# Kernel tuning notes

Measured on AMD Instinct MI355X. Metric: run time of the kernel, lower is better.

## Reference

```python
import jax, jax.numpy as jnp
import numpy as np

N_NODES = 100000
N_EDGES = 640000
HIDDEN = 128
OUT = 128


def _graph_conv(x, edge_index, W_rel, b_rel, W_root):
    # PyG GraphConv (aggr='add'):
    #   out[i] = x[i] @ W_root.T + (sum_{(j->i) in E} x[j]) @ W_rel.T + b_rel
    src, dst = edge_index[0], edge_index[1]
    agg = jax.ops.segment_sum(x[src], dst, num_segments=N_NODES)  # [N, d_in]
    return x @ W_root.T + agg @ W_rel.T + b_rel


def setup_inputs() -> dict:
    key = jax.random.key(0)
    ks = jax.random.split(key, 10)
    x = jax.random.normal(ks[0], (N_NODES, HIDDEN), dtype=jnp.float32)
    edge_index = jax.random.randint(ks[1], (2, N_EDGES), 0, N_NODES, dtype=jnp.int64)
    s = 1.0 / np.sqrt(HIDDEN)
    def w(k, o, i):
        return jax.random.normal(k, (o, i), dtype=jnp.float32) * s
    return {
        "x": x,
        "edge_index": edge_index,
        "W_rel0": w(ks[2], HIDDEN, HIDDEN), "b0": jnp.zeros((HIDDEN,), jnp.float32), "W_root0": w(ks[3], HIDDEN, HIDDEN),
        "W_rel1": w(ks[4], HIDDEN, HIDDEN), "b1": jnp.zeros((HIDDEN,), jnp.float32), "W_root1": w(ks[5], HIDDEN, HIDDEN),
        "W_rel2": w(ks[6], OUT, HIDDEN),    "b2": jnp.zeros((OUT,), jnp.float32),    "W_root2": w(ks[7], OUT, HIDDEN),
    }


def reference(x, edge_index, W_rel0, b0, W_root0, W_rel1, b1, W_root1, W_rel2, b2, W_root2):
    h = jax.nn.relu(_graph_conv(x, edge_index, W_rel0, b0, W_root0))
    h = jax.nn.relu(_graph_conv(h, edge_index, W_rel1, b1, W_root1))
    h = _graph_conv(h, edge_index, W_rel2, b2, W_root2)  # no ReLU on end_conv
    return h
```

## Files before the change

### kernel.cpp

```cpp
#include <hip/hip_runtime.h>

constexpr int HID = 128;

typedef __attribute__((ext_vector_type(8))) short bf16x8;
typedef __attribute__((ext_vector_type(4))) float f32x4;

__device__ __forceinline__ unsigned short f2bf(float f) {
    unsigned int u = __float_as_uint(f);
    u += 0x7fffu + ((u >> 16) & 1u);
    return (unsigned short)(u >> 16);
}
__device__ __forceinline__ float bf_lo(unsigned int v) { return __uint_as_float(v << 16); }
__device__ __forceinline__ float bf_hi(unsigned int v) { return __uint_as_float(v & 0xffff0000u); }

__device__ __forceinline__ void gload16(const void* g, void* l) {
    __builtin_amdgcn_global_load_lds(
        (const __attribute__((address_space(1))) void*)g,
        (__attribute__((address_space(3))) void*)l, 16, 0, 0);
}

__global__ __launch_bounds__(256) void cvt_x_k(
    const float* __restrict__ in, unsigned short* __restrict__ out, int n4)
{
    const int i = blockIdx.x * 256 + threadIdx.x;
    if (i >= n4) return;
    const float4 v = reinterpret_cast<const float4*>(in)[i];
    ushort4 o;
    o.x = f2bf(v.x); o.y = f2bf(v.y); o.z = f2bf(v.z); o.w = f2bf(v.w);
    reinterpret_cast<ushort4*>(out)[i] = o;
}

struct WPtrs { const float* s[6]; unsigned short* d[6]; };
__global__ __launch_bounds__(256) void cvt_w_k(WPtrs p)
{
    const int which = blockIdx.y;
    const int i = blockIdx.x * 256 + threadIdx.x;
    if (i >= (HID * HID) / 4) return;
    const float4 v = reinterpret_cast<const float4*>(p.s[which])[i];
    ushort4 o;
    o.x = f2bf(v.x); o.y = f2bf(v.y); o.z = f2bf(v.z); o.w = f2bf(v.w);
    reinterpret_cast<ushort4*>(p.d[which])[i] = o;
}

__global__ __launch_bounds__(256) void hist_k(
    const int* __restrict__ dst, int* __restrict__ deg, int nEdges)
{
    const int i = blockIdx.x * blockDim.x + threadIdx.x;
    if (i < nEdges) atomicAdd(&deg[dst[i]], 1);
}

__global__ __launch_bounds__(256) void scan1_k(
    const int* __restrict__ deg, int* __restrict__ part,
    int* __restrict__ blockSums, int n)
{
    __shared__ int s[256];
    const int t = threadIdx.x;
    const int i = blockIdx.x * 1024 + t * 4;
    const int e0 = (i + 0 < n) ? deg[i + 0] : 0;
    const int e1 = (i + 1 < n) ? deg[i + 1] : 0;
    const int e2 = (i + 2 < n) ? deg[i + 2] : 0;
    const int e3 = (i + 3 < n) ? deg[i + 3] : 0;
    const int local = e0 + e1 + e2 + e3;
    s[t] = local;
    __syncthreads();
    for (int off = 1; off < 256; off <<= 1) {
        int v = 0;
        if (t >= off) v = s[t - off];
        __syncthreads();
        if (t >= off) s[t] += v;
        __syncthreads();
    }
    const int incl = s[t];
    int excl = incl - local;
    if (t == 255) blockSums[blockIdx.x] = incl;
    if (i + 0 < n) part[i + 0] = excl; excl += e0;
    if (i + 1 < n) part[i + 1] = excl; excl += e1;
    if (i + 2 < n) part[i + 2] = excl; excl += e2;
    if (i + 3 < n) part[i + 3] = excl;
}

__global__ __launch_bounds__(128) void scan2_k(int* __restrict__ blockSums, int nb)
{
    __shared__ int s[128];
    const int t = threadIdx.x;
    const int v = (t < nb) ? blockSums[t] : 0;
    s[t] = v;
    __syncthreads();
    for (int off = 1; off < 128; off <<= 1) {
        int u = 0;
        if (t >= off) u = s[t - off];
        __syncthreads();
        if (t >= off) s[t] += u;
        __syncthreads();
    }
    if (t < nb) blockSums[t] = s[t] - v;
}

__global__ __launch_bounds__(256) void scan3_k(
    const int* __restrict__ part, const int* __restrict__ blockSums,
    int* __restrict__ rowStart, int* __restrict__ cursor, int n, int nEdges)
{
    const int i = blockIdx.x * blockDim.x + threadIdx.x;
    if (i < n) {
        const int v = part[i] + blockSums[i >> 10];
        rowStart[i] = v;
        cursor[i]   = v;
    }
    if (i == n) rowStart[n] = nEdges;
}

__global__ __launch_bounds__(256) void fill_k(
    const int* __restrict__ src, const int* __restrict__ dst,
    int* __restrict__ cursor, int* __restrict__ eSrc, int nEdges)
{
    const int i = blockIdx.x * blockDim.x + threadIdx.x;
    if (i < nEdges) {
        const int pos = atomicAdd(&cursor[dst[i]], 1);
        eSrc[pos] = src[i];
    }
}

__global__ __launch_bounds__(256) void gather_agg_k(
    const unsigned short* __restrict__ feat,
    const int*            __restrict__ rowStart,
    const int*            __restrict__ eSrc,
    unsigned short*       __restrict__ agg,
    int nNodes)
{
    const int node = (int)((blockIdx.x * blockDim.x + threadIdx.x) >> 6);
    if (node >= nNodes) return;
    const int lane = threadIdx.x & 63;
    const int beg = rowStart[node];
    const int end = rowStart[node + 1];
    const size_t colOff = (size_t)lane * 2;

    float ax = 0.f, ay = 0.f;

    for (int base = beg; base < end; base += 64) {
        const int cnt = min(64, end - base);
        const int si = eSrc[base + min(lane, cnt - 1)];

        int j = 0;
        for (; j + 8 <= cnt; j += 8) {
            unsigned int v[8];
#pragma unroll
            for (int q = 0; q < 8; ++q) {
                const int s = __shfl(si, j + q, 64);
                v[q] = *reinterpret_cast<const unsigned int*>(feat + (size_t)s * HID + colOff);
            }
#pragma unroll
            for (int q = 0; q < 8; ++q) { ax += bf_lo(v[q]); ay += bf_hi(v[q]); }
        }
        if (j + 4 <= cnt) {
            unsigned int v[4];
#pragma unroll
            for (int q = 0; q < 4; ++q) {
                const int s = __shfl(si, j + q, 64);
                v[q] = *reinterpret_cast<const unsigned int*>(feat + (size_t)s * HID + colOff);
            }
#pragma unroll
            for (int q = 0; q < 4; ++q) { ax += bf_lo(v[q]); ay += bf_hi(v[q]); }
            j += 4;
        }
        if (j + 2 <= cnt) {
            const int s0 = __shfl(si, j, 64);
            const int s1 = __shfl(si, j + 1, 64);
            const unsigned int v0 = *reinterpret_cast<const unsigned int*>(feat + (size_t)s0 * HID + colOff);
            const unsigned int v1 = *reinterpret_cast<const unsigned int*>(feat + (size_t)s1 * HID + colOff);
            ax += bf_lo(v0) + bf_lo(v1);
            ay += bf_hi(v0) + bf_hi(v1);
            j += 2;
        }
        if (j < cnt) {
            const int s = __shfl(si, j, 64);
            const unsigned int v = *reinterpret_cast<const unsigned int*>(feat + (size_t)s * HID + colOff);
            ax += bf_lo(v);
            ay += bf_hi(v);
        }
    }

    const unsigned int packed = (unsigned int)f2bf(ax) | ((unsigned int)f2bf(ay) << 16);
    *reinterpret_cast<unsigned int*>(agg + (size_t)node * HID + colOff) = packed;
}

__device__ __forceinline__ void stage_tile(
    const unsigned short* __restrict__ F, const unsigned short* __restrict__ Wm,
    unsigned short* XsBuf, unsigned short* WsBuf,
    int w, int stHalf, int rsub, int srcColB, int k0, int row0, int rowMax)
{
    if (w < 2) {
#pragma unroll
        for (int q = 0; q < 8; ++q) {
            const int row = stHalf * 64 + q * 8 + rsub;
            const int gr  = min(row0 + row, rowMax);
            gload16((const char*)(F + (size_t)gr * HID + k0) + srcColB,
                    XsBuf + (stHalf * 64 + q * 8) * 64);
        }
    } else {
#pragma unroll
        for (int q = 0; q < 8; ++q) {
            const int row = stHalf * 64 + q * 8 + rsub;
            gload16((const char*)(Wm + (size_t)row * HID + k0) + srcColB,
                    WsBuf + (stHalf * 64 + q * 8) * 64);
        }
    }
}

template <int MODE>
__global__ __launch_bounds__(256) void gemm_mfma_k(
    const unsigned short* __restrict__ X,
    const unsigned short* __restrict__ AGG,
    const unsigned short* __restrict__ Wroot,
    const unsigned short* __restrict__ Wrel,
    const float*          __restrict__ bias,
    void*                 __restrict__ OUTv,
    int nRows)
{
    __shared__ unsigned short Xs[2][128 * 64];
    __shared__ unsigned short Ws[2][128 * 64];

    const int tid  = threadIdx.x;
    const int lane = tid & 63;
    const int w    = tid >> 6;
    const int row0 = blockIdx.x * 128;

    const int wr = w >> 1, wc = w & 1;
    const int R0 = wr * 64, C0 = wc * 64;
    const int lr = lane & 15, lk = lane >> 4;
    const int swz = (lr & 7) << 4;

    const int rsub    = lane >> 3;
    const int srcColB = (((lane & 7) ^ rsub) << 4);
    const int stHalf  = w & 1;
    const int rowMax  = nRows - 1;

    f32x4 acc[4][4];
#pragma unroll
    for (int m = 0; m < 4; ++m)
#pragma unroll
        for (int n = 0; n < 4; ++n) acc[m][n] = f32x4{0.f, 0.f, 0.f, 0.f};

    stage_tile(X, Wroot, Xs[0], Ws[0], w, stHalf, rsub, srcColB, 0, row0, rowMax);

#pragma unroll
    for (int t = 0; t < 4; ++t) {
        const int cur = t & 1;
        if (t < 3) {
            const unsigned short* Fn = (t + 1 < 2) ? X : AGG;
            const unsigned short* Wn = (t + 1 < 2) ? Wroot : Wrel;
            stage_tile(Fn, Wn, Xs[cur ^ 1], Ws[cur ^ 1],
                       w, stHalf, rsub, srcColB, ((t + 1) & 1) * 64, row0, rowMax);
            asm volatile("s_waitcnt vmcnt(8)" ::: "memory");
        } else {
            asm volatile("s_waitcnt vmcnt(0)" ::: "memory");
        }
        __builtin_amdgcn_s_barrier();

#pragma unroll
        for (int ks = 0; ks < 2; ++ks) {
            bf16x8 af[4], bfr[4];
            const int kB = (ks * 64 + lk * 16) ^ swz;
#pragma unroll
            for (int m = 0; m < 4; ++m) {
                const int row = R0 + m * 16 + lr;
                af[m] = *reinterpret_cast<const bf16x8*>((const char*)Xs[cur] + row * 128 + kB);
            }
#pragma unroll
            for (int n = 0; n < 4; ++n) {
                const int col = C0 + n * 16 + lr;
                bfr[n] = *reinterpret_cast<const bf16x8*>((const char*)Ws[cur] + col * 128 + kB);
            }
#pragma unroll
            for (int m = 0; m < 4; ++m)
#pragma unroll
                for (int n = 0; n < 4; ++n)
                    acc[m][n] = __builtin_amdgcn_mfma_f32_16x16x32_bf16(
                        af[m], bfr[n], acc[m][n], 0, 0, 0);
        }
        if (t < 3) __builtin_amdgcn_s_barrier();
    }

    float bv[4];
#pragma unroll
    for (int n = 0; n < 4; ++n) bv[n] = bias[C0 + n * 16 + lr];

#pragma unroll
    for (int m = 0; m < 4; ++m) {
        const int rbase = row0 + R0 + m * 16 + lk * 4;
#pragma unroll
        for (int j = 0; j < 4; ++j) {
            const int r = rbase + j;
            if (r < nRows) {
#pragma unroll
                for (int n = 0; n < 4; ++n) {
                    const int col = C0 + n * 16 + lr;
                    float v = acc[m][n][j] + bv[n];
                    if (MODE == 0) {
                        v = fmaxf(v, 0.f);
                        ((unsigned short*)OUTv)[(size_t)r * HID + col] = f2bf(v);
                    } else {
                        ((float*)OUTv)[(size_t)r * HID + col] = v;
                    }
                }
            }
        }
    }
}

extern "C" void kernel_launch(void* const* d_in, const int* in_sizes, int n_in,
                              void* d_out, int out_size, void* d_ws, size_t ws_size,
                              hipStream_t stream)
{
    const float* x      = (const float*)d_in[0];
    const int*   ei     = (const int*)  d_in[1];
    const float* Wrel0  = (const float*)d_in[2];
    const float* b0     = (const float*)d_in[3];
    const float* Wroot0 = (const float*)d_in[4];
    const float* Wrel1  = (const float*)d_in[5];
    const float* b1     = (const float*)d_in[6];
    const float* Wroot1 = (const float*)d_in[7];
    const float* Wrel2  = (const float*)d_in[8];
    const float* b2     = (const float*)d_in[9];
    const float* Wroot2 = (const float*)d_in[10];

    const int nNodes = in_sizes[0] / HID;
    const int nEdges = in_sizes[1] / 2;
    const int* srcI = ei;
    const int* dstI = ei + nEdges;
    const size_t nF = (size_t)nNodes * HID;

    float* OUT = (float*)d_out;

    unsigned short* xb   = (unsigned short*)d_ws;
    unsigned short* hA   = xb + nF;
    unsigned short* hB   = hA + nF;
    unsigned short* aggb = hB + nF;
    unsigned short* wb   = aggb + nF;
    int* deg       = (int*)(wb + 6 * HID * HID);
    int* part      = deg + nNodes;
    int* rowStart  = part + nNodes;
    int* cursor    = rowStart + nNodes + 1;
    int* blockSums = cursor + nNodes;
    int* eSrc      = blockSums + 128;

    unsigned short* Wrel0b  = wb + 0 * HID * HID;
    unsigned short* Wroot0b = wb + 1 * HID * HID;
    unsigned short* Wrel1b  = wb + 2 * HID * HID;
    unsigned short* Wroot1b = wb + 3 * HID * HID;
    unsigned short* Wrel2b  = wb + 4 * HID * HID;
    unsigned short* Wroot2b = wb + 5 * HID * HID;

    cvt_x_k<<<(int)((nF / 4 + 255) / 256), 256, 0, stream>>>(x, xb, (int)(nF / 4));
    WPtrs wp;
    wp.s[0] = Wrel0;  wp.d[0] = Wrel0b;
    wp.s[1] = Wroot0; wp.d[1] = Wroot0b;
    wp.s[2] = Wrel1;  wp.d[2] = Wrel1b;
    wp.s[3] = Wroot1; wp.d[3] = Wroot1b;
    wp.s[4] = Wrel2;  wp.d[4] = Wrel2b;
    wp.s[5] = Wroot2; wp.d[5] = Wroot2b;
    cvt_w_k<<<dim3(16, 6), 256, 0, stream>>>(wp);

    const int nb = (nNodes + 1023) / 1024;
    hipMemsetAsync(deg, 0, (size_t)nNodes * sizeof(int), stream);
    hist_k<<<(nEdges + 255) / 256, 256, 0, stream>>>(dstI, deg, nEdges);
    scan1_k<<<nb, 256, 0, stream>>>(deg, part, blockSums, nNodes);
    scan2_k<<<1, 128, 0, stream>>>(blockSums, nb);
    scan3_k<<<(nNodes + 256) / 256, 256, 0, stream>>>(part, blockSums, rowStart, cursor, nNodes, nEdges);
    fill_k<<<(nEdges + 255) / 256, 256, 0, stream>>>(srcI, dstI, cursor, eSrc, nEdges);

    const int aGrid = (int)(((size_t)nNodes * 64 + 255) / 256);
    const int gGrid = (nNodes + 127) / 128;

    gather_agg_k<<<aGrid, 256, 0, stream>>>(xb, rowStart, eSrc, aggb, nNodes);
    gemm_mfma_k<0><<<gGrid, 256, 0, stream>>>(xb, aggb, Wroot0b, Wrel0b, b0, hA, nNodes);

    gather_agg_k<<<aGrid, 256, 0, stream>>>(hA, rowStart, eSrc, aggb, nNodes);
    gemm_mfma_k<0><<<gGrid, 256, 0, stream>>>(hA, aggb, Wroot1b, Wrel1b, b1, hB, nNodes);

    gather_agg_k<<<aGrid, 256, 0, stream>>>(hB, rowStart, eSrc, aggb, nNodes);
    gemm_mfma_k<1><<<gGrid, 256, 0, stream>>>(hB, aggb, Wroot2b, Wrel2b, b2, OUT, nNodes);
}
```

Measured before the change: 244.4 us.

## Gather with 16-lane groups and 16-byte loads; record edge rank during histogram

The aggregation kernel now assigns four nodes per wavefront, each handled by a 16-lane group that loads 16-byte chunks (8 bf16 values) per lane. The old layout had one node per wavefront with 4-byte loads. This is meant to cut load instruction count and idle lanes for low-degree nodes. CSR construction now records each edge's atomic rank in the histogram pass, so the fill pass writes without a second atomic. The trade-off is an extra rank array in memory and more registers per lane for accumulators.

```diff
diff --git a/kernel.cpp b/kernel.cpp
--- a/kernel.cpp
+++ b/kernel.cpp
@@ -42,11 +42,12 @@
     reinterpret_cast<ushort4*>(p.d[which])[i] = o;
 }
 
-__global__ __launch_bounds__(256) void hist_k(
-    const int* __restrict__ dst, int* __restrict__ deg, int nEdges)
+__global__ __launch_bounds__(256) void hist_rank_k(
+    const int* __restrict__ dst, int* __restrict__ deg,
+    int* __restrict__ rank, int nEdges)
 {
     const int i = blockIdx.x * blockDim.x + threadIdx.x;
-    if (i < nEdges) atomicAdd(&deg[dst[i]], 1);
+    if (i < nEdges) rank[i] = atomicAdd(&deg[dst[i]], 1);
 }
 
 __global__ __launch_bounds__(256) void scan1_k(
@@ -98,26 +99,20 @@
 
 __global__ __launch_bounds__(256) void scan3_k(
     const int* __restrict__ part, const int* __restrict__ blockSums,
-    int* __restrict__ rowStart, int* __restrict__ cursor, int n, int nEdges)
+    int* __restrict__ rowStart, int n, int nEdges)
 {
     const int i = blockIdx.x * blockDim.x + threadIdx.x;
-    if (i < n) {
-        const int v = part[i] + blockSums[i >> 10];
-        rowStart[i] = v;
-        cursor[i]   = v;
-    }
+    if (i < n) rowStart[i] = part[i] + blockSums[i >> 10];
     if (i == n) rowStart[n] = nEdges;
 }
 
-__global__ __launch_bounds__(256) void fill_k(
+__global__ __launch_bounds__(256) void fill2_k(
     const int* __restrict__ src, const int* __restrict__ dst,
-    int* __restrict__ cursor, int* __restrict__ eSrc, int nEdges)
+    const int* __restrict__ rank, const int* __restrict__ rowStart,
+    int* __restrict__ eSrc, int nEdges)
 {
     const int i = blockIdx.x * blockDim.x + threadIdx.x;
-    if (i < nEdges) {
-        const int pos = atomicAdd(&cursor[dst[i]], 1);
-        eSrc[pos] = src[i];
-    }
+    if (i < nEdges) eSrc[rowStart[dst[i]] + rank[i]] = src[i];
 }
 
 __global__ __launch_bounds__(256) void gather_agg_k(
@@ -127,60 +122,90 @@
     unsigned short*       __restrict__ agg,
     int nNodes)
 {
-    const int node = (int)((blockIdx.x * blockDim.x + threadIdx.x) >> 6);
+    const int wid  = (blockIdx.x * blockDim.x + threadIdx.x) >> 6;
+    const int lane = threadIdx.x & 63;
+    const int g    = lane >> 4;
+    const int sl   = lane & 15;
+    const int node = wid * 4 + g;
     if (node >= nNodes) return;
-    const int lane = threadIdx.x & 63;
+
     const int beg = rowStart[node];
     const int end = rowStart[node + 1];
-    const size_t colOff = (size_t)lane * 2;
-
-    float ax = 0.f, ay = 0.f;
-
-    for (int base = beg; base < end; base += 64) {
-        const int cnt = min(64, end - base);
-        const int si = eSrc[base + min(lane, cnt - 1)];
+    const size_t colOff = (size_t)sl * 8;
+    const int gbase = g << 4;
+
+    float acc[8];
+#pragma unroll
+    for (int q = 0; q < 8; ++q) acc[q] = 0.f;
+
+    for (int base = beg; base < end; base += 16) {
+        const int cnt = min(16, end - base);
+        const int si = eSrc[base + min(sl, cnt - 1)];
 
         int j = 0;
         for (; j + 8 <= cnt; j += 8) {
-            unsigned int v[8];
+            uint4 v[8];
 #pragma unroll
             for (int q = 0; q < 8; ++q) {
-                const int s = __shfl(si, j + q, 64);
-                v[q] = *reinterpret_cast<const unsigned int*>(feat + (size_t)s * HID + colOff);
-            }
-#pragma unroll
-            for (int q = 0; q < 8; ++q) { ax += bf_lo(v[q]); ay += bf_hi(v[q]); }
+                const int s = __shfl(si, gbase + j + q, 64);
+                v[q] = *reinterpret_cast<const uint4*>(feat + (size_t)s * HID + colOff);
+            }
+#pragma unroll
+            for (int q = 0; q < 8; ++q) {
+                acc[0] += bf_lo(v[q].x); acc[1] += bf_hi(v[q].x);
+                acc[2] += bf_lo(v[q].y); acc[3] += bf_hi(v[q].y);
+                acc[4] += bf_lo(v[q].z); acc[5] += bf_hi(v[q].z);
+                acc[6] += bf_lo(v[q].w); acc[7] += bf_hi(v[q].w);
+            }
         }
         if (j + 4 <= cnt) {
-            unsigned int v[4];
+            uint4 v[4];
 #pragma unroll
             for (int q = 0; q < 4; ++q) {
-                const int s = __shfl(si, j + q, 64);
-                v[q] = *reinterpret_cast<const unsigned int*>(feat + (size_t)s * HID + colOff);
-            }
-#pragma unroll
-            for (int q = 0; q < 4; ++q) { ax += bf_lo(v[q]); ay += bf_hi(v[q]); }
+                const int s = __shfl(si, gbase + j + q, 64);
+                v[q] = *reinterpret_cast<const uint4*>(feat + (size_t)s * HID + colOff);
+            }
+#pragma unroll
+            for (int q = 0; q < 4; ++q) {
+                acc[0] += bf_lo(v[q].x); acc[1] += bf_hi(v[q].x);
+                acc[2] += bf_lo(v[q].y); acc[3] += bf_hi(v[q].y);
+                acc[4] += bf_lo(v[q].z); acc[5] += bf_hi(v[q].z);
+                acc[6] += bf_lo(v[q].w); acc[7] += bf_hi(v[q].w);
+            }
             j += 4;
         }
         if (j + 2 <= cnt) {
-            const int s0 = __shfl(si, j, 64);
-            const int s1 = __shfl(si, j + 1, 64);
-            const unsigned int v0 = *reinterpret_cast<const unsigned int*>(feat + (size_t)s0 * HID + colOff);
-            const unsigned int v1 = *reinterpret_cast<const unsigned int*>(feat + (size_t)s1 * HID + colOff);
-            ax += bf_lo(v0) + bf_lo(v1);
-            ay += bf_hi(v0) + bf_hi(v1);
+            uint4 v[2];
+#pragma unroll
+            for (int q = 0; q < 2; ++q) {
+                const int s = __shfl(si, gbase + j + q, 64);
+                v[q] = *reinterpret_cast<const uint4*>(feat + (size_t)s * HID + colOff);
+            }
+#pragma unroll
+            for (int q = 0; q < 2; ++q) {
+                acc[0] += bf_lo(v[q].x); acc[1] += bf_hi(v[q].x);
+                acc[2] += bf_lo(v[q].y); acc[3] += bf_hi(v[q].y);
+                acc[4] += bf_lo(v[q].z); acc[5] += bf_hi(v[q].z);
+                acc[6] += bf_lo(v[q].w); acc[7] += bf_hi(v[q].w);
+            }
             j += 2;
         }
         if (j < cnt) {
-            const int s = __shfl(si, j, 64);
-            const unsigned int v = *reinterpret_cast<const unsigned int*>(feat + (size_t)s * HID + colOff);
-            ax += bf_lo(v);
-            ay += bf_hi(v);
-        }
-    }
-
-    const unsigned int packed = (unsigned int)f2bf(ax) | ((unsigned int)f2bf(ay) << 16);
-    *reinterpret_cast<unsigned int*>(agg + (size_t)node * HID + colOff) = packed;
+            const int s = __shfl(si, gbase + j, 64);
+            const uint4 v = *reinterpret_cast<const uint4*>(feat + (size_t)s * HID + colOff);
+            acc[0] += bf_lo(v.x); acc[1] += bf_hi(v.x);
+            acc[2] += bf_lo(v.y); acc[3] += bf_hi(v.y);
+            acc[4] += bf_lo(v.z); acc[5] += bf_hi(v.z);
+            acc[6] += bf_lo(v.w); acc[7] += bf_hi(v.w);
+        }
+    }
+
+    uint4 o;
+    o.x = (unsigned int)f2bf(acc[0]) | ((unsigned int)f2bf(acc[1]) << 16);
+    o.y = (unsigned int)f2bf(acc[2]) | ((unsigned int)f2bf(acc[3]) << 16);
+    o.z = (unsigned int)f2bf(acc[4]) | ((unsigned int)f2bf(acc[5]) << 16);
+    o.w = (unsigned int)f2bf(acc[6]) | ((unsigned int)f2bf(acc[7]) << 16);
+    *reinterpret_cast<uint4*>(agg + (size_t)node * HID + colOff) = o;
 }
 
 __device__ __forceinline__ void stage_tile(
@@ -339,9 +364,9 @@
     int* deg       = (int*)(wb + 6 * HID * HID);
     int* part      = deg + nNodes;
     int* rowStart  = part + nNodes;
-    int* cursor    = rowStart + nNodes + 1;
-    int* blockSums = cursor + nNodes;
-    int* eSrc      = blockSums + 128;
+    int* blockSums = rowStart + nNodes + 1;
+    int* rank      = blockSums + 128;
+    int* eSrc      = rank + nEdges;
 
     unsigned short* Wrel0b  = wb + 0 * HID * HID;
     unsigned short* Wroot0b = wb + 1 * HID * HID;
@@ -362,13 +387,13 @@
 
     const int nb = (nNodes + 1023) / 1024;
     hipMemsetAsync(deg, 0, (size_t)nNodes * sizeof(int), stream);
-    hist_k<<<(nEdges + 255) / 256, 256, 0, stream>>>(dstI, deg, nEdges);
+    hist_rank_k<<<(nEdges + 255) / 256, 256, 0, stream>>>(dstI, deg, rank, nEdges);
     scan1_k<<<nb, 256, 0, stream>>>(deg, part, blockSums, nNodes);
     scan2_k<<<1, 128, 0, stream>>>(blockSums, nb);
-    scan3_k<<<(nNodes + 256) / 256, 256, 0, stream>>>(part, blockSums, rowStart, cursor, nNodes, nEdges);
-    fill_k<<<(nEdges + 255) / 256, 256, 0, stream>>>(srcI, dstI, cursor, eSrc, nEdges);
-
-    const int aGrid = (int)(((size_t)nNodes * 64 + 255) / 256);
+    scan3_k<<<(nNodes + 256) / 256, 256, 0, stream>>>(part, blockSums, rowStart, nNodes, nEdges);
+    fill2_k<<<(nEdges + 255) / 256, 256, 0, stream>>>(srcI, dstI, rank, rowStart, eSrc, nEdges);
+
+    const int aGrid = (int)(((size_t)(nNodes + 3) / 4 * 64 + 255) / 256);
     const int gGrid = (nNodes + 127) / 128;
 
     gather_agg_k<<<aGrid, 256, 0, stream>>>(xb, rowStart, eSrc, aggb, nNodes);
```

After: 206.8 us. 1.18x faster.
